# Kernel optimization log

Measured on AMD Instinct MI355X. Metric: run time of the kernel, lower is better.

Reference implementation:

```python
import jax, jax.numpy as jnp
import numpy as np
from jax import lax

DT = 0.001          # integration step
SCALE = 0.2         # hopf_input_scale
NUM_STEPS = 5       # Euler sub-steps per sequence position
MU = 1.0            # Hopf limit-cycle radius^2


def hopf_layer(h, omega):
    """Hopf oscillator bank driven by h: [B, T, U]; omega: [U] (rad/s).
    For each sequence position, run NUM_STEPS Euler steps of
      dx = (mu - (x^2+y^2)) x - omega*y + scale*u
      dy = (mu - (x^2+y^2)) y + omega*x
    carrying (x, y) state across positions. Returns per-position states
    (z_real, z_imag), each [B, T, U]."""

    def per_timestep(state, u):  # u: [B, U]
        def euler(c, _):
            x, y = c
            r2 = x * x + y * y
            nx = x + DT * ((MU - r2) * x - omega * y + SCALE * u)
            ny = y + DT * ((MU - r2) * y + omega * x)
            return (nx, ny), None
        state, _ = lax.scan(euler, state, None, length=NUM_STEPS)
        return state, state

    B, T, U = h.shape
    z0 = (jnp.zeros((B, U), h.dtype), jnp.zeros((B, U), h.dtype))
    _, (xs, ys) = lax.scan(per_timestep, z0, jnp.swapaxes(h, 0, 1))  # [T,B,U]
    return jnp.swapaxes(xs, 0, 1), jnp.swapaxes(ys, 0, 1)


def setup_inputs() -> dict:
    key = jax.random.key(0)
    ks = jax.random.split(key, 12)
    B, T = 128, 1024
    V, E, U, P, C = 50000, 100, 100, 20, 2
    two_pi = 2.0 * np.pi
    return {
        "x": jax.random.randint(ks[0], (B, T), 0, V),
        "emb": jax.random.normal(ks[1], (V, E), jnp.float32) * 0.05,
        "omega1": jax.random.uniform(ks[2], (U,), jnp.float32, two_pi * 1.0, two_pi * 15.0),
        "omega2": jax.random.uniform(ks[3], (U,), jnp.float32, two_pi * 1.0, two_pi * 15.0),
        "w1": jax.random.normal(ks[4], (2 * U, U), jnp.float32) * 0.07,
        "b1": jnp.zeros((U,), jnp.float32),
        "w2": jax.random.normal(ks[5], (2 * U, U), jnp.float32) * 0.07,
        "b2": jnp.zeros((U,), jnp.float32),
        "wp": jax.random.normal(ks[6], (U, P), jnp.float32) * 0.1,
        "bp": jnp.zeros((P,), jnp.float32),
        "wh": jax.random.normal(ks[7], (P, C), jnp.float32) * 0.2,
        "bh": jnp.zeros((C,), jnp.float32),
    }


def reference(x, emb, omega1, omega2, w1, b1, w2, b2, wp, bp, wh, bh):
    h0 = emb[x]                                   # [B, T, E]
    z1r, z1i = hopf_layer(h0, omega1)             # [B, T, U] each
    h1 = jax.nn.relu(jnp.concatenate([z1r, z1i], axis=2) @ w1 + b1)
    z2r, z2i = hopf_layer(h1, omega2)
    h2 = jax.nn.relu(jnp.concatenate([z2r, z2i], axis=2) @ w2 + b2)
    last = h2[:, -1, :]                           # many-to-one: last timestep
    h3 = jnp.tanh(last @ wp + bp)                 # [B, P]
    return h3 @ wh + bh                           # [B, C]
```

## Files before the change

### kernel.cpp

```cpp
#include <hip/hip_runtime.h>
#include <cmath>

namespace {
constexpr int T = 1024, BATCH = 128, U = 100, E = 100, P = 20, C = 2;
constexpr int TC = 64, NC = 16;
constexpr float DT = 0.001f, SCALE = 0.2f, MU = 1.0f;
constexpr float DTS = DT * SCALE;

constexpr uint32_t WROW = 464u, ZROW = 464u, EROW = 128u, HROW = 128u;
constexpr uint32_t WLB = 0u;
constexpr uint32_t ZBB = 46400u, ZBUF = 29696u;
constexpr uint32_t EBB = 105792u, EBUF = 12800u;
constexpr uint32_t HBB = 131392u, HBUF = 12800u;
constexpr uint32_t ARENA = 156992u;

typedef _Float16 f16x8 __attribute__((ext_vector_type(8)));
typedef _Float16 f16x4 __attribute__((ext_vector_type(4)));
typedef float f32x4 __attribute__((ext_vector_type(4)));
typedef _Float16 h2_t __attribute__((ext_vector_type(2)));

__device__ __forceinline__ void eul5(float& xx, float& yy, float dom, float ax) {
    constexpr float c0 = 1.0f + DT * MU;
#pragma unroll
    for (int s = 0; s < 5; ++s) {
        float r2 = fmaf(yy, yy, xx * xx);
        float sc = fmaf(-DT, r2, c0);
        float nx = fmaf(xx, sc, fmaf(-dom, yy, ax));
        float ny = fmaf(yy, sc, dom * xx);
        xx = nx; yy = ny;
    }
}

__launch_bounds__(512, 1)
__global__ void donn_kernel(const int* __restrict__ xg,
                            const float* __restrict__ emb,
                            const float* __restrict__ omega1,
                            const float* __restrict__ omega2,
                            const float* __restrict__ w1,
                            const float* __restrict__ b1,
                            const float* __restrict__ w2,
                            const float* __restrict__ b2,
                            const float* __restrict__ wp,
                            const float* __restrict__ bp,
                            const float* __restrict__ wh,
                            const float* __restrict__ bh,
                            float* __restrict__ out)
{
    const int b = blockIdx.x;
    const int tid = threadIdx.x;

    __shared__ __align__(16) char smem[ARENA];
    __shared__ int xs[2][TC];
    __shared__ float zf2[2][104];
    __shared__ float pb[2][104];
    __shared__ float h2s[104];
    __shared__ float h3s[32];

    float x1 = 0.f, y1 = 0.f, x2 = 0.f, y2 = 0.f;
    float dom1 = 0.f, dom2 = 0.f;
    int jc = 0, j2c = 0;
    bool act1 = false;
    int mw = 0, lane = 0, mh = 0, n0 = 0;
    float b1r[4] = {0.f, 0.f, 0.f, 0.f};
    uint32_t brow[4] = {0u, 0u, 0u, 0u};

    if (tid < 128) {
        jc = (tid < U) ? tid : (U - 1);
        act1 = tid < U;
        dom1 = DT * omega1[jc];
    } else if (tid < 256) {
        const int j2 = tid - 128;
        j2c = (j2 < U) ? j2 : (U - 1);
        dom2 = DT * omega2[j2c];
    } else {
        mw = (tid >> 6) - 4;
        lane = tid & 63;
        mh = mw >> 1;
        n0 = (mw & 1) * 4;
#pragma unroll
        for (int n = 0; n < 4; ++n) {
            int j = (n0 + n) * 16 + (lane & 15);
            int jj = (j < U) ? j : (U - 1);
            b1r[n] = b1[jj];
            brow[n] = WLB + (uint32_t)jj * WROW + 16u * (uint32_t)(lane >> 4);
        }
    }

    if (tid < TC) xs[0][tid] = xg[b * T + tid];
    else if (tid < 2 * TC) xs[1][tid - TC] = xg[b * T + TC + (tid - TC)];
    for (int idx = tid; idx < 200 * 100; idx += 512) {
        int k = idx / 100, j = idx - 100 * k;
        int kp = (k < U) ? (2 * k) : (2 * (k - U) + 1);
        *(_Float16*)(smem + WLB + (uint32_t)j * WROW + 2u * (uint32_t)kp) = (_Float16)w1[k * U + j];
    }
    for (int idx = tid; idx < 100 * 16; idx += 512) {
        int row = idx >> 4, wd = idx & 15;
        *(float*)(smem + WLB + (uint32_t)row * WROW + 400u + 4u * (uint32_t)wd) = 0.f;
    }
    for (int idx = tid; idx < 128 * 16; idx += 512) {
        int zr = idx >> 4, wd = idx & 15;
        uint32_t base = ZBB + (uint32_t)(zr >> 6) * ZBUF + (uint32_t)(zr & 63) * ZROW;
        *(float*)(smem + base + 400u + 4u * (uint32_t)wd) = 0.f;
    }
    __syncthreads();
    for (int idx = tid; idx < 100 * TC; idx += 512) {
        int j = idx >> 6, t = idx & 63;
        int tok = xs[0][t];
        uint32_t off = EBB + (uint32_t)j * EROW
                     + (uint32_t)(((((t >> 3) ^ (j & 7))) << 4) + 2 * (t & 7));
        *(_Float16*)(smem + off) = (_Float16)emb[tok * E + j];
    }
    __syncthreads();

    for (int p = 0; p <= NC + 1; ++p) {
        if (tid < 128) {
            if (tid < TC && p + 2 < NC)
                xs[p & 1][tid] = xg[b * T + (p + 2) * TC + tid];
            if (p < NC) {
                const uint32_t q = (uint32_t)(p & 1);
                const char* ebase = smem + EBB + q * EBUF + (uint32_t)jc * EROW;
                char* zbase = smem + ZBB + q * ZBUF + 4u * (uint32_t)jc;
                const int s = jc & 7;
                f16x8 eA = *(const f16x8*)(ebase + ((0 ^ s) << 4));
                for (int gg = 0; gg < 4; ++gg) {
                    f16x8 eB = *(const f16x8*)(ebase + (((2 * gg + 1) ^ s) << 4));
                    {
                        char* zt = zbase + (uint32_t)(16 * gg) * ZROW;
#pragma unroll
                        for (int i = 0; i < 8; ++i) {
                            eul5(x1, y1, dom1, DTS * (float)eA[i]);
                            if (act1) {
                                h2_t zz; zz[0] = (_Float16)x1; zz[1] = (_Float16)y1;
                                *(h2_t*)(zt + (uint32_t)i * ZROW) = zz;
                            }
                        }
                    }
                    if (gg < 3) eA = *(const f16x8*)(ebase + (((2 * gg + 2) ^ s) << 4));
                    {
                        char* zt = zbase + (uint32_t)(16 * gg + 8) * ZROW;
#pragma unroll
                        for (int i = 0; i < 8; ++i) {
                            eul5(x1, y1, dom1, DTS * (float)eB[i]);
                            if (act1) {
                                h2_t zz; zz[0] = (_Float16)x1; zz[1] = (_Float16)y1;
                                *(h2_t*)(zt + (uint32_t)i * ZROW) = zz;
                            }
                        }
                    }
                }
            }
        } else if (tid < 256) {
            if (p >= 2) {
                const uint32_t q = (uint32_t)(p & 1);
                const char* hbase = smem + HBB + q * HBUF + (uint32_t)j2c * HROW;
                const int s = j2c & 7;
                f16x8 eA = *(const f16x8*)(hbase + ((0 ^ s) << 4));
                for (int gg = 0; gg < 4; ++gg) {
                    f16x8 eB = *(const f16x8*)(hbase + (((2 * gg + 1) ^ s) << 4));
#pragma unroll
                    for (int i = 0; i < 8; ++i)
                        eul5(x2, y2, dom2, DTS * (float)eA[i]);
                    if (gg < 3) eA = *(const f16x8*)(hbase + (((2 * gg + 2) ^ s) << 4));
#pragma unroll
                    for (int i = 0; i < 8; ++i)
                        eul5(x2, y2, dom2, DTS * (float)eB[i]);
                }
            }
        } else {
            float er[25];
            const bool edo = (p + 1 < NC);
            if (edo) {
                const uint32_t qe = (uint32_t)((p + 1) & 1);
                int tok = xs[qe][lane];
                const float* ep = emb + (size_t)tok * E;
#pragma unroll
                for (int i = 0; i < 25; ++i) er[i] = ep[mw * 25 + i];
            }
            if (p >= 1 && p <= NC) {
                const uint32_t qm = (uint32_t)((p - 1) & 1);
                const char* zb = smem + ZBB + qm * ZBUF;
                f32x4 acc[2][4];
#pragma unroll
                for (int mt = 0; mt < 2; ++mt)
#pragma unroll
                    for (int n = 0; n < 4; ++n) acc[mt][n] = (f32x4)0.f;
#pragma unroll
                for (int mt = 0; mt < 2; ++mt) {
                    const uint32_t ar = (uint32_t)(mh * 32 + mt * 16 + (lane & 15)) * ZROW
                                        + 16u * (uint32_t)(lane >> 4);
                    f16x8 af[7];
#pragma unroll
                    for (int ks = 0; ks < 7; ++ks)
                        af[ks] = *(const f16x8*)(zb + ar + 64u * ks);
#pragma unroll
                    for (int n = 0; n < 4; ++n)
#pragma unroll
                        for (int ks = 0; ks < 7; ++ks) {
                            f16x8 bf = *(const f16x8*)(smem + brow[n] + 64u * ks);
                            acc[mt][n] = __builtin_amdgcn_mfma_f32_16x16x32_f16(
                                af[ks], bf, acc[mt][n], 0, 0, 0);
                        }
                }
                char* hb = smem + HBB + qm * HBUF;
#pragma unroll
                for (int mt = 0; mt < 2; ++mt)
#pragma unroll
                    for (int n = 0; n < 4; ++n) {
                        const int j = (n0 + n) * 16 + (lane & 15);
                        if (j < U) {
                            const int t0v = mh * 32 + mt * 16 + (lane >> 4) * 4;
                            f16x4 hv;
#pragma unroll
                            for (int r = 0; r < 4; ++r)
                                hv[r] = (_Float16)fmaxf(acc[mt][n][r] + b1r[n], 0.f);
                            uint32_t off = (uint32_t)j * HROW
                                + (uint32_t)(((((t0v >> 3) ^ (j & 7))) << 4) + ((2 * t0v) & 15));
                            *(f16x4*)(hb + off) = hv;
                        }
                    }
            }
            if (edo) {
                const uint32_t qe = (uint32_t)((p + 1) & 1);
                char* eb = smem + EBB + qe * EBUF;
#pragma unroll
                for (int i = 0; i < 25; ++i) {
                    int jrow = mw * 25 + i;
                    uint32_t off = (uint32_t)jrow * EROW
                        + (uint32_t)(((((lane >> 3) ^ (jrow & 7))) << 4) + 2 * (lane & 7));
                    *(_Float16*)(eb + off) = (_Float16)er[i];
                }
            }
        }
        __syncthreads();
    }

    if (tid >= 128 && tid < 256) {
        const int j = tid - 128;
        if (j < U) { zf2[0][j] = x2; zf2[1][j] = y2; }
    }
    __syncthreads();

    if (tid >= 256 && tid < 456) {
        const int e = tid - 256;
        const int h = e / 100, jq = e - 100 * (e / 100);
        float acc2 = 0.f;
#pragma unroll 4
        for (int kk = 0; kk < 100; ++kk)
            acc2 = fmaf(zf2[h][kk], w2[(100 * h + kk) * U + jq], acc2);
        pb[h][jq] = acc2;
    }
    __syncthreads();

    if (tid < U) h2s[tid] = fmaxf(pb[0][tid] + pb[1][tid] + b2[tid], 0.f);
    __syncthreads();

    if (tid < P) {
        float acc = bp[tid];
#pragma unroll 4
        for (int j = 0; j < U; ++j) acc = fmaf(h2s[j], wp[j * P + tid], acc);
        h3s[tid] = tanhf(acc);
    }
    __syncthreads();

    if (tid < C) {
        float acc = bh[tid];
#pragma unroll
        for (int pp = 0; pp < P; ++pp) acc = fmaf(h3s[pp], wh[pp * C + tid], acc);
        out[b * C + tid] = acc;
    }
}
}

extern "C" void kernel_launch(void* const* d_in, const int* in_sizes, int n_in,
                              void* d_out, int out_size, void* d_ws, size_t ws_size,
                              hipStream_t stream) {
    const int* xi        = (const int*)d_in[0];
    const float* emb     = (const float*)d_in[1];
    const float* omega1  = (const float*)d_in[2];
    const float* omega2  = (const float*)d_in[3];
    const float* w1      = (const float*)d_in[4];
    const float* b1      = (const float*)d_in[5];
    const float* w2      = (const float*)d_in[6];
    const float* b2      = (const float*)d_in[7];
    const float* wp      = (const float*)d_in[8];
    const float* bp      = (const float*)d_in[9];
    const float* wh      = (const float*)d_in[10];
    const float* bh      = (const float*)d_in[11];
    float* out           = (float*)d_out;

    hipLaunchKernelGGL(donn_kernel, dim3(BATCH), dim3(512), 0, stream,
                       xi, emb, omega1, omega2, w1, b1, w2, b2, wp, bp, wh, bh, out);
}
```

Before: 127.9 us.

## Carry r² recurrence in Euler loop and switch GEMM to 32x32x16 MFMA

The Euler step now updates r² through an algebraic recurrence (r²' = (sc²+ω²dt²)r² + 2a·sc·x − 2a·dt·ω·y + a²), which takes the r² computation off the x/y dependency chain. The oscillator loops are restructured into a single 8-group loop that prefetches the next input vector two groups ahead. The layer-1 projection GEMM is rewritten from 16x16x32 to 32x32x16 MFMA tiles, which reduces A-fragment reloads and changes the output layout. The z store base now uses tid rather than the clamped index. The recurrence can accumulate rounding drift relative to directly recomputing x²+y².

```diff
diff --git a/kernel.cpp b/kernel.cpp
--- a/kernel.cpp
+++ b/kernel.cpp
@@ -16,17 +16,26 @@
 
 typedef _Float16 f16x8 __attribute__((ext_vector_type(8)));
 typedef _Float16 f16x4 __attribute__((ext_vector_type(4)));
-typedef float f32x4 __attribute__((ext_vector_type(4)));
+typedef float f32x16 __attribute__((ext_vector_type(16)));
 typedef _Float16 h2_t __attribute__((ext_vector_type(2)));
 
-__device__ __forceinline__ void eul5(float& xx, float& yy, float dom, float ax) {
+__device__ __forceinline__ void eul5r(float& xx, float& yy, float& r2,
+                                      float dom, float domsq, float ax) {
     constexpr float c0 = 1.0f + DT * MU;
+    const float tax = ax + ax;
+    const float ax2 = ax * ax;
+    const float n2ad = -tax * dom;
 #pragma unroll
     for (int s = 0; s < 5; ++s) {
-        float r2 = fmaf(yy, yy, xx * xx);
         float sc = fmaf(-DT, r2, c0);
-        float nx = fmaf(xx, sc, fmaf(-dom, yy, ax));
+        float s2 = fmaf(sc, sc, domsq);
+        float g  = tax * xx;
+        float h  = fmaf(n2ad, yy, ax2);
+        float inner = fmaf(sc, g, h);
+        float wx = fmaf(-dom, yy, ax);
+        float nx = fmaf(xx, sc, wx);
         float ny = fmaf(yy, sc, dom * xx);
+        r2 = fmaf(s2, r2, inner);
         xx = nx; yy = ny;
     }
 }
@@ -56,33 +65,36 @@
     __shared__ float h2s[104];
     __shared__ float h3s[32];
 
-    float x1 = 0.f, y1 = 0.f, x2 = 0.f, y2 = 0.f;
-    float dom1 = 0.f, dom2 = 0.f;
+    float x1 = 0.f, y1 = 0.f, r21 = 0.f;
+    float x2 = 0.f, y2 = 0.f, r22 = 0.f;
+    float dom1 = 0.f, dom2 = 0.f, dsq1 = 0.f, dsq2 = 0.f;
     int jc = 0, j2c = 0;
     bool act1 = false;
-    int mw = 0, lane = 0, mh = 0, n0 = 0;
-    float b1r[4] = {0.f, 0.f, 0.f, 0.f};
-    uint32_t brow[4] = {0u, 0u, 0u, 0u};
+    int lane = 0, mh = 0, np = 0, mw = 0;
+    float b1r[2] = {0.f, 0.f};
+    uint32_t brow[2] = {0u, 0u};
 
     if (tid < 128) {
         jc = (tid < U) ? tid : (U - 1);
         act1 = tid < U;
         dom1 = DT * omega1[jc];
+        dsq1 = dom1 * dom1;
     } else if (tid < 256) {
         const int j2 = tid - 128;
         j2c = (j2 < U) ? j2 : (U - 1);
         dom2 = DT * omega2[j2c];
+        dsq2 = dom2 * dom2;
     } else {
         mw = (tid >> 6) - 4;
         lane = tid & 63;
         mh = mw >> 1;
-        n0 = (mw & 1) * 4;
-#pragma unroll
-        for (int n = 0; n < 4; ++n) {
-            int j = (n0 + n) * 16 + (lane & 15);
+        np = mw & 1;
+#pragma unroll
+        for (int nt = 0; nt < 2; ++nt) {
+            int j = np * 64 + nt * 32 + (lane & 31);
             int jj = (j < U) ? j : (U - 1);
-            b1r[n] = b1[jj];
-            brow[n] = WLB + (uint32_t)jj * WROW + 16u * (uint32_t)(lane >> 4);
+            b1r[nt] = b1[jj];
+            brow[nt] = WLB + (uint32_t)jj * WROW + 16u * (uint32_t)(lane >> 5);
         }
     }
 
@@ -119,34 +131,23 @@
             if (p < NC) {
                 const uint32_t q = (uint32_t)(p & 1);
                 const char* ebase = smem + EBB + q * EBUF + (uint32_t)jc * EROW;
-                char* zbase = smem + ZBB + q * ZBUF + 4u * (uint32_t)jc;
+                char* zbase = smem + ZBB + q * ZBUF + 4u * (uint32_t)tid;
                 const int s = jc & 7;
-                f16x8 eA = *(const f16x8*)(ebase + ((0 ^ s) << 4));
-                for (int gg = 0; gg < 4; ++gg) {
-                    f16x8 eB = *(const f16x8*)(ebase + (((2 * gg + 1) ^ s) << 4));
-                    {
-                        char* zt = zbase + (uint32_t)(16 * gg) * ZROW;
-#pragma unroll
-                        for (int i = 0; i < 8; ++i) {
-                            eul5(x1, y1, dom1, DTS * (float)eA[i]);
-                            if (act1) {
-                                h2_t zz; zz[0] = (_Float16)x1; zz[1] = (_Float16)y1;
-                                *(h2_t*)(zt + (uint32_t)i * ZROW) = zz;
-                            }
+                f16x8 e0 = *(const f16x8*)(ebase + ((0 ^ s) << 4));
+                f16x8 e1 = *(const f16x8*)(ebase + ((1 ^ s) << 4));
+                for (int gg = 0; gg < 8; ++gg) {
+                    f16x8 e2 = e1;
+                    if (gg + 2 < 8) e2 = *(const f16x8*)(ebase + (((gg + 2) ^ s) << 4));
+                    char* zt = zbase + (uint32_t)(8 * gg) * ZROW;
+#pragma unroll
+                    for (int i = 0; i < 8; ++i) {
+                        eul5r(x1, y1, r21, dom1, dsq1, DTS * (float)e0[i]);
+                        if (act1) {
+                            h2_t zz; zz[0] = (_Float16)x1; zz[1] = (_Float16)y1;
+                            *(h2_t*)(zt + (uint32_t)i * ZROW) = zz;
                         }
                     }
-                    if (gg < 3) eA = *(const f16x8*)(ebase + (((2 * gg + 2) ^ s) << 4));
-                    {
-                        char* zt = zbase + (uint32_t)(16 * gg + 8) * ZROW;
-#pragma unroll
-                        for (int i = 0; i < 8; ++i) {
-                            eul5(x1, y1, dom1, DTS * (float)eB[i]);
-                            if (act1) {
-                                h2_t zz; zz[0] = (_Float16)x1; zz[1] = (_Float16)y1;
-                                *(h2_t*)(zt + (uint32_t)i * ZROW) = zz;
-                            }
-                        }
-                    }
+                    e0 = e1; e1 = e2;
                 }
             }
         } else if (tid < 256) {
@@ -154,16 +155,15 @@
                 const uint32_t q = (uint32_t)(p & 1);
                 const char* hbase = smem + HBB + q * HBUF + (uint32_t)j2c * HROW;
                 const int s = j2c & 7;
-                f16x8 eA = *(const f16x8*)(hbase + ((0 ^ s) << 4));
-                for (int gg = 0; gg < 4; ++gg) {
-                    f16x8 eB = *(const f16x8*)(hbase + (((2 * gg + 1) ^ s) << 4));
+                f16x8 e0 = *(const f16x8*)(hbase + ((0 ^ s) << 4));
+                f16x8 e1 = *(const f16x8*)(hbase + ((1 ^ s) << 4));
+                for (int gg = 0; gg < 8; ++gg) {
+                    f16x8 e2 = e1;
+                    if (gg + 2 < 8) e2 = *(const f16x8*)(hbase + (((gg + 2) ^ s) << 4));
 #pragma unroll
                     for (int i = 0; i < 8; ++i)
-                        eul5(x2, y2, dom2, DTS * (float)eA[i]);
-                    if (gg < 3) eA = *(const f16x8*)(hbase + (((2 * gg + 2) ^ s) << 4));
-#pragma unroll
-                    for (int i = 0; i < 8; ++i)
-                        eul5(x2, y2, dom2, DTS * (float)eB[i]);
+                        eul5r(x2, y2, r22, dom2, dsq2, DTS * (float)e0[i]);
+                    e0 = e1; e1 = e2;
                 }
             }
         } else {
@@ -179,45 +179,37 @@
             if (p >= 1 && p <= NC) {
                 const uint32_t qm = (uint32_t)((p - 1) & 1);
                 const char* zb = smem + ZBB + qm * ZBUF;
-                f32x4 acc[2][4];
-#pragma unroll
-                for (int mt = 0; mt < 2; ++mt)
-#pragma unroll
-                    for (int n = 0; n < 4; ++n) acc[mt][n] = (f32x4)0.f;
-#pragma unroll
-                for (int mt = 0; mt < 2; ++mt) {
-                    const uint32_t ar = (uint32_t)(mh * 32 + mt * 16 + (lane & 15)) * ZROW
-                                        + 16u * (uint32_t)(lane >> 4);
-                    f16x8 af[7];
-#pragma unroll
-                    for (int ks = 0; ks < 7; ++ks)
-                        af[ks] = *(const f16x8*)(zb + ar + 64u * ks);
-#pragma unroll
-                    for (int n = 0; n < 4; ++n)
-#pragma unroll
-                        for (int ks = 0; ks < 7; ++ks) {
-                            f16x8 bf = *(const f16x8*)(smem + brow[n] + 64u * ks);
-                            acc[mt][n] = __builtin_amdgcn_mfma_f32_16x16x32_f16(
-                                af[ks], bf, acc[mt][n], 0, 0, 0);
-                        }
+                const uint32_t arow = (uint32_t)(mh * 32 + (lane & 31)) * ZROW
+                                      + 16u * (uint32_t)(lane >> 5);
+                f32x16 acc0 = (f32x16)0.f, acc1 = (f32x16)0.f;
+#pragma unroll
+                for (int ks = 0; ks < 14; ++ks) {
+                    f16x8 af = *(const f16x8*)(zb + arow + 32u * ks);
+                    f16x8 bf0 = *(const f16x8*)(smem + brow[0] + 32u * ks);
+                    acc0 = __builtin_amdgcn_mfma_f32_32x32x16_f16(af, bf0, acc0, 0, 0, 0);
+                    f16x8 bf1 = *(const f16x8*)(smem + brow[1] + 32u * ks);
+                    acc1 = __builtin_amdgcn_mfma_f32_32x32x16_f16(af, bf1, acc1, 0, 0, 0);
                 }
                 char* hb = smem + HBB + qm * HBUF;
 #pragma unroll
-                for (int mt = 0; mt < 2; ++mt)
-#pragma unroll
-                    for (int n = 0; n < 4; ++n) {
-                        const int j = (n0 + n) * 16 + (lane & 15);
-                        if (j < U) {
-                            const int t0v = mh * 32 + mt * 16 + (lane >> 4) * 4;
+                for (int nt = 0; nt < 2; ++nt) {
+                    const int j = np * 64 + nt * 32 + (lane & 31);
+                    if (j < U) {
+#pragma unroll
+                        for (int g = 0; g < 4; ++g) {
+                            const int tb = mh * 32 + 8 * g + 4 * (lane >> 5);
                             f16x4 hv;
 #pragma unroll
-                            for (int r = 0; r < 4; ++r)
-                                hv[r] = (_Float16)fmaxf(acc[mt][n][r] + b1r[n], 0.f);
+                            for (int r = 0; r < 4; ++r) {
+                                float v = (nt == 0) ? acc0[4 * g + r] : acc1[4 * g + r];
+                                hv[r] = (_Float16)fmaxf(v + b1r[nt], 0.f);
+                            }
                             uint32_t off = (uint32_t)j * HROW
-                                + (uint32_t)(((((t0v >> 3) ^ (j & 7))) << 4) + ((2 * t0v) & 15));
+                                + (uint32_t)(((((tb >> 3) ^ (j & 7))) << 4) + ((2 * tb) & 15));
                             *(f16x4*)(hb + off) = hv;
                         }
                     }
+                }
             }
             if (edo) {
                 const uint32_t qe = (uint32_t)((p + 1) & 1);
```

Measured after the change: 157.9 us. 23.5% more time.
